# Performance work log

Measured on AMD Instinct MI355X. Metric: run time of the kernel, lower is better.

## Reference

```python
import jax, jax.numpy as jnp
import numpy as np

H = 8          # num heads
HD = 64        # head dim
DV = 512       # values_dim
DC = 128       # coords_dim
DI = 512       # att_inner_dim
DF = 2048      # mlp inner dim


def _ln(x, g, b, eps=1e-5):
    mu = jnp.mean(x, -1, keepdims=True)
    var = jnp.mean((x - mu) ** 2, -1, keepdims=True)
    return (x - mu) * jax.lax.rsqrt(var + eps) * g + b


def _rms(x, g, eps=1e-6):
    return x * jax.lax.rsqrt(jnp.mean(x * x, -1, keepdims=True) + eps) * g


def _heads(x):  # b n (h d) -> b h n d
    b, n, _ = x.shape
    return x.reshape(b, n, H, HD).transpose(0, 2, 1, 3)


def setup_inputs() -> dict:
    key = jax.random.key(0)
    ks = iter(jax.random.split(key, 40))
    r = lambda shape, s=0.02: jax.random.normal(next(ks), shape, jnp.float32) * s
    inp = {
        'coords': jax.random.normal(next(ks), (4, 4096, DC), jnp.float32),
        'values': jax.random.normal(next(ks), (4, 4096, DV), jnp.float32),
        'Lv': jax.random.normal(next(ks), (4, 1024, DV), jnp.float32),
        'Lc': jax.random.normal(next(ks), (4, 1024, DC), jnp.float32),
        'lam': jax.random.normal(next(ks), (1,), jnp.float32),
        'lvn_g': jnp.ones((DV,)), 'lvn_b': jnp.zeros((DV,)),
        'lcn_g': jnp.ones((DC,)), 'lcn_b': jnp.zeros((DC,)),
        'ck_w': r((DC, DI)), 'ck_b': jnp.zeros((DI,)), 'ck_g': jnp.ones((DI,)),
        'cq_w': r((DC, DI)), 'cq_b': jnp.zeros((DI,)), 'cq_g': jnp.ones((DI,)),
        'vq_w': r((DV, DI)), 'vq_b': jnp.zeros((DI,)), 'vq_g': jnp.ones((DI,)),
        'vk_w': r((DV, 2 * DI)), 'vk_b': jnp.zeros((2 * DI,)),
        'op_w': r((DI, DV)), 'op_b': jnp.zeros((DV,)),
        'oln_g': jnp.ones((DV,)), 'oln_b': jnp.zeros((DV,)),
        'm1_w': r((DV, DF)), 'm1_b': jnp.zeros((DF,)),
        'm2_w': r((DF, DF)), 'm2_b': jnp.zeros((DF,)),
        'm3_w': r((DF, DV)), 'm3_b': jnp.zeros((DV,)),
    }
    return inp


def reference(coords, values, Lv, Lc, lam, lvn_g, lvn_b, lcn_g, lcn_b,
              ck_w, ck_b, ck_g, cq_w, cq_b, cq_g, vq_w, vq_b, vq_g,
              vk_w, vk_b, op_w, op_b, oln_g, oln_b,
              m1_w, m1_b, m2_w, m2_b, m3_w, m3_b):
    Lv = _ln(Lv, lvn_g, lvn_b)
    Lc = _ln(Lc, lcn_g, lcn_b)
    vk = Lv @ vk_w + vk_b                     # [b, nl, 2*DI]
    v_v, k_v = jnp.split(vk, 2, axis=-1)
    k_c = _rms(Lc @ ck_w + ck_b, ck_g)
    k_c, v_v, k_v = _heads(k_c), _heads(v_v), _heads(k_v)  # [b,h,nl,d]
    q_v = _heads(_rms(values @ vq_w + vq_b, vq_g))         # [b,h,nq,d]
    q_c = _heads(_rms(coords @ cq_w + cq_b, cq_g))
    # dual-score attention
    scores = jnp.einsum('bhnd,bhmd->bhnm', q_c, k_c) \
        + lam[0] * jnp.einsum('bhnd,bhmd->bhnm', q_v, k_v)
    scores = scores / np.float32(np.sqrt(HD))
    attn = jax.nn.softmax(scores, axis=-1)
    V_out = jnp.einsum('bhnm,bhmd->bhnd', attn, v_v)       # [b,h,nq,d]
    b, _, nq, _ = V_out.shape
    V_out = V_out.transpose(0, 2, 1, 3).reshape(b, nq, DI)
    V_out = V_out @ op_w + op_b
    # (LayerNorm, MLP) head: Linear-GELU-Linear-GELU-Linear
    h = _ln(V_out, oln_g, oln_b)
    h = jax.nn.gelu(h @ m1_w + m1_b)
    h = jax.nn.gelu(h @ m2_w + m2_b)
    return h @ m3_w + m3_b
```

## Files before the change

### kernel.cpp

```cpp
#include <hip/hip_runtime.h>
#include <cstdint>
#include <cstddef>

typedef __bf16 bf16_t;
typedef __bf16 bf16x8 __attribute__((ext_vector_type(8)));
typedef __bf16 bf16x4 __attribute__((ext_vector_type(4)));
typedef float  f32x4  __attribute__((ext_vector_type(4)));

typedef __attribute__((address_space(1))) void gvoid_t;
typedef __attribute__((address_space(3))) void lvoid_t;

__device__ __forceinline__ f32x4 mfma16(bf16x8 a, bf16x8 b, f32x4 c) {
  return __builtin_amdgcn_mfma_f32_16x16x32_bf16(a, b, c, 0, 0, 0);
}

__device__ __forceinline__ void async_copy16(const void* g, void* l) {
  __builtin_amdgcn_global_load_lds((gvoid_t*)g, (lvoid_t*)l, 16, 0, 0);
}

__device__ __forceinline__ float gelu_tanh(float x) {
  float u = 0.7978845608028654f * (x + 0.044715f * x * x * x);
  float e = exp2f(2.8853900817779268f * u);
  float t = 1.f - 2.f / (e + 1.f);
  return 0.5f * x * (1.f + t);
}

struct TransBatch {
  const float* src[8];
  bf16_t* dst[8];
  int K[8], N[8], bx[8], base[8];
};

__global__ void transpose_batch_kernel(TransBatch d) {
  int id = blockIdx.x;
  int mi = 0;
#pragma unroll
  for (int j = 1; j < 8; j++)
    if (id >= d.base[j]) mi = j;
  int local = id - d.base[mi];
  int bxw = d.bx[mi];
  int n0 = (local % bxw) * 32, k0 = (local / bxw) * 32;
  const float* in = d.src[mi];
  bf16_t* out = d.dst[mi];
  int K = d.K[mi], N = d.N[mi];

  __shared__ float t[32][33];
  int tx = threadIdx.x, ty = threadIdx.y;
#pragma unroll
  for (int i = 0; i < 4; i++)
    t[ty + i * 8][tx] = in[(size_t)(k0 + ty + i * 8) * N + n0 + tx];
  __syncthreads();
#pragma unroll
  for (int i = 0; i < 4; i++)
    out[(size_t)(n0 + ty + i * 8) * K + k0 + tx] = (bf16_t)t[tx][ty + i * 8];
}

__global__ void transpose_v_kernel(const bf16_t* __restrict__ vk, bf16_t* __restrict__ vt) {
  __shared__ bf16_t t[32][33];
  int b = blockIdx.z;
  int d0 = blockIdx.x * 32, m0 = blockIdx.y * 32;
  int tx = threadIdx.x, ty = threadIdx.y;
#pragma unroll
  for (int i = 0; i < 4; i++)
    t[ty + i * 8][tx] = vk[((size_t)b * 1024 + m0 + ty + i * 8) * 1024 + d0 + tx];
  __syncthreads();
#pragma unroll
  for (int i = 0; i < 4; i++)
    vt[((size_t)b * 512 + d0 + ty + i * 8) * 1024 + m0 + tx] = t[tx][ty + i * 8];
}

__global__ void cvt2_bf16_kernel(const float* __restrict__ a, bf16_t* __restrict__ oa, int n4a,
                                 const float* __restrict__ b, bf16_t* __restrict__ ob, int n4b) {
  int i = blockIdx.x * blockDim.x + threadIdx.x;
  const float* s;
  bf16_t* o;
  int j;
  if (i < n4a) { s = a; o = oa; j = i; }
  else { j = i - n4a; if (j >= n4b) return; s = b; o = ob; }
  float4 v = ((const float4*)s)[j];
  bf16x4 r = {(bf16_t)v.x, (bf16_t)v.y, (bf16_t)v.z, (bf16_t)v.w};
  ((bf16x4*)o)[j] = r;
}

template <int D>
__global__ void ln_kernel(const float* __restrict__ x, const float* __restrict__ g,
                          const float* __restrict__ bb, bf16_t* __restrict__ out) {
  int row = blockIdx.x, t = threadIdx.x;
  float v = x[(size_t)row * D + t];
  float s = v, s2 = v * v;
#pragma unroll
  for (int o = 32; o > 0; o >>= 1) { s += __shfl_xor(s, o); s2 += __shfl_xor(s2, o); }
  __shared__ float rs[8], rs2[8];
  constexpr int NW = D / 64;
  int w = t >> 6;
  if ((t & 63) == 0) { rs[w] = s; rs2[w] = s2; }
  __syncthreads();
  if (t < 64) {
    float a = (t < NW) ? rs[t] : 0.f;
    float a2 = (t < NW) ? rs2[t] : 0.f;
#pragma unroll
    for (int o = 4; o > 0; o >>= 1) { a += __shfl_xor(a, o); a2 += __shfl_xor(a2, o); }
    if (t == 0) { rs[0] = a; rs2[0] = a2; }
  }
  __syncthreads();
  float mu = rs[0] * (1.f / D);
  float var = rs2[0] * (1.f / D) - mu * mu;
  float rr = rsqrtf(var + 1e-5f);
  out[(size_t)row * D + t] = (bf16_t)((v - mu) * rr * g[t] + bb[t]);
}

__global__ void rms_kernel(const float* __restrict__ x, const float* __restrict__ g,
                           bf16_t* __restrict__ out) {
  int row = blockIdx.x, t = threadIdx.x;
  float v = x[(size_t)row * 512 + t];
  float s2 = v * v;
#pragma unroll
  for (int o = 32; o > 0; o >>= 1) s2 += __shfl_xor(s2, o);
  __shared__ float rs2[8];
  int w = t >> 6;
  if ((t & 63) == 0) rs2[w] = s2;
  __syncthreads();
  if (t < 64) {
    float a = (t < 8) ? rs2[t] : 0.f;
#pragma unroll
    for (int o = 4; o > 0; o >>= 1) a += __shfl_xor(a, o);
    if (t == 0) rs2[0] = a;
  }
  __syncthreads();
  float r = rsqrtf(rs2[0] * (1.f / 512.f) + 1e-6f);
  out[(size_t)row * 512 + t] = (bf16_t)(v * r * g[t]);
}

template <int EPI>
__global__ __launch_bounds__(256, 2) void gemm_bt(
    const bf16_t* __restrict__ A, const bf16_t* __restrict__ Bt,
    const float* __restrict__ bias, void* __restrict__ outp,
    int M, int N, int K) {
  __shared__ __align__(16) bf16_t As[128 * 32];
  __shared__ __align__(16) bf16_t Bs[128 * 32];
  const int tid = threadIdx.x;
  const int lane = tid & 63, wv = tid >> 6;
  const int quad = lane >> 4, l16 = lane & 15;
  const int m_base = blockIdx.y * 128, n_base = blockIdx.x * 128;
  const int wm = wv & 1, wn = wv >> 1;
  f32x4 acc[4][4] = {};

  for (int k0 = 0; k0 < K; k0 += 32) {
#pragma unroll
    for (int c = 0; c < 2; c++) {
      int p = c * 256 + tid;
      int row = p >> 2;
      int kc = (p & 3) ^ ((row >> 1) & 3);
      async_copy16(&A[(size_t)(m_base + row) * K + k0 + kc * 8], &As[(size_t)p * 8]);
      async_copy16(&Bt[(size_t)(n_base + row) * K + k0 + kc * 8], &Bs[(size_t)p * 8]);
    }
    __syncthreads();
    bf16x8 af[4], bfr[4];
#pragma unroll
    for (int mi = 0; mi < 4; mi++) {
      int r = wm * 64 + mi * 16 + l16;
      int kc = quad ^ ((r >> 1) & 3);
      af[mi] = *(const bf16x8*)&As[(size_t)(r * 4 + kc) * 8];
    }
#pragma unroll
    for (int ni = 0; ni < 4; ni++) {
      int r = wn * 64 + ni * 16 + l16;
      int kc = quad ^ ((r >> 1) & 3);
      bfr[ni] = *(const bf16x8*)&Bs[(size_t)(r * 4 + kc) * 8];
    }
#pragma unroll
    for (int mi = 0; mi < 4; mi++)
#pragma unroll
      for (int ni = 0; ni < 4; ni++)
        acc[mi][ni] = mfma16(af[mi], bfr[ni], acc[mi][ni]);
    __syncthreads();
  }

#pragma unroll
  for (int mi = 0; mi < 4; mi++) {
    int m = m_base + wm * 64 + mi * 16 + quad * 4;
#pragma unroll
    for (int ni = 0; ni < 4; ni++) {
      int n = n_base + wn * 64 + ni * 16 + l16;
      float bv = bias[n];
#pragma unroll
      for (int r2 = 0; r2 < 4; r2++) {
        float v = acc[mi][ni][r2] + bv;
        if (EPI == 2) v = gelu_tanh(v);
        if (EPI == 0) ((float*)outp)[(size_t)(m + r2) * N + n] = v;
        else          ((bf16_t*)outp)[(size_t)(m + r2) * N + n] = (bf16_t)v;
      }
    }
  }
}

template <int EPI>
__global__ __launch_bounds__(256, 2) void gemm64(
    const bf16_t* __restrict__ A, const bf16_t* __restrict__ Bt,
    const float* __restrict__ bias, void* __restrict__ outp,
    int M, int N, int K) {
  __shared__ __align__(16) bf16_t As[64 * 32];
  __shared__ __align__(16) bf16_t Bs[128 * 32];
  const int tid = threadIdx.x;
  const int lane = tid & 63, wv = tid >> 6;
  const int quad = lane >> 4, l16 = lane & 15;
  const int m_base = blockIdx.y * 64, n_base = blockIdx.x * 128;
  const int wm = wv & 1, wn = wv >> 1;
  f32x4 acc[2][4] = {};

  for (int k0 = 0; k0 < K; k0 += 32) {
    {
      int p = tid;
      int row = p >> 2;
      int kc = (p & 3) ^ ((row >> 1) & 3);
      async_copy16(&A[(size_t)(m_base + row) * K + k0 + kc * 8], &As[(size_t)p * 8]);
    }
#pragma unroll
    for (int c = 0; c < 2; c++) {
      int p = c * 256 + tid;
      int row = p >> 2;
      int kc = (p & 3) ^ ((row >> 1) & 3);
      async_copy16(&Bt[(size_t)(n_base + row) * K + k0 + kc * 8], &Bs[(size_t)p * 8]);
    }
    __syncthreads();
    bf16x8 af[2], bfr[4];
#pragma unroll
    for (int mi = 0; mi < 2; mi++) {
      int r = wm * 32 + mi * 16 + l16;
      int kc = quad ^ ((r >> 1) & 3);
      af[mi] = *(const bf16x8*)&As[(size_t)(r * 4 + kc) * 8];
    }
#pragma unroll
    for (int ni = 0; ni < 4; ni++) {
      int r = wn * 64 + ni * 16 + l16;
      int kc = quad ^ ((r >> 1) & 3);
      bfr[ni] = *(const bf16x8*)&Bs[(size_t)(r * 4 + kc) * 8];
    }
#pragma unroll
    for (int mi = 0; mi < 2; mi++)
#pragma unroll
      for (int ni = 0; ni < 4; ni++)
        acc[mi][ni] = mfma16(af[mi], bfr[ni], acc[mi][ni]);
    __syncthreads();
  }

#pragma unroll
  for (int mi = 0; mi < 2; mi++) {
    int m = m_base + wm * 32 + mi * 16 + quad * 4;
#pragma unroll
    for (int ni = 0; ni < 4; ni++) {
      int n = n_base + wn * 64 + ni * 16 + l16;
      float bv = bias[n];
#pragma unroll
      for (int r2 = 0; r2 < 4; r2++) {
        float v = acc[mi][ni][r2] + bv;
        if (EPI == 2) v = gelu_tanh(v);
        if (EPI == 0) ((float*)outp)[(size_t)(m + r2) * N + n] = v;
        else          ((bf16_t*)outp)[(size_t)(m + r2) * N + n] = (bf16_t)v;
      }
    }
  }
}

__global__ __launch_bounds__(256, 2) void attn_kernel(
    const bf16_t* __restrict__ qc, const bf16_t* __restrict__ qv,
    const bf16_t* __restrict__ kcb, const bf16_t* __restrict__ vkb,
    const bf16_t* __restrict__ vt, const float* __restrict__ lamp,
    bf16_t* __restrict__ vout) {
  const int b = blockIdx.z, h = blockIdx.y;
  const int tid = threadIdx.x;
  const int lane = tid & 63, wv = tid >> 6;
  const int quad = lane >> 4, l16 = lane & 15;
  const int qrow0 = blockIdx.x * 128 + wv * 32;
  const float SCL = 0.125f * 1.4426950408889634f;
  const float C1 = SCL, C2 = lamp[0] * SCL;

  __shared__ __align__(16) bf16_t kcS[64 * 64];
  __shared__ __align__(16) bf16_t kvS[64 * 64];
  __shared__ __align__(16) bf16_t vtS[64 * 64];
  __shared__ __align__(16) bf16_t sP[4][32 * 64];
  bf16_t* sPw = sP[wv];

  bf16x8 qcf[2][2], qvf[2][2];
#pragma unroll
  for (int mt = 0; mt < 2; mt++)
#pragma unroll
    for (int ks = 0; ks < 2; ks++) {
      size_t o = ((size_t)b * 4096 + qrow0 + mt * 16 + l16) * 512 + h * 64 + ks * 32 + quad * 8;
      qcf[mt][ks] = *(const bf16x8*)&qc[o];
      qvf[mt][ks] = *(const bf16x8*)&qv[o];
    }

  f32x4 O[2][4] = {};
  float ls[2][4] = {};

  for (int kb = 0; kb < 16; kb++) {
#pragma unroll
    for (int i = 0; i < 2; i++) {
      int p = i * 256 + tid;
      int row = p >> 3;
      int gc = (p & 7) ^ (row & 7);
      async_copy16(&kcb[((size_t)b * 1024 + kb * 64 + row) * 512 + h * 64 + gc * 8],
                   &kcS[(size_t)p * 8]);
      async_copy16(&vkb[((size_t)b * 1024 + kb * 64 + row) * 1024 + 512 + h * 64 + gc * 8],
                   &kvS[(size_t)p * 8]);
      async_copy16(&vt[((size_t)((b * 8 + h) * 64) + row) * 1024 + kb * 64 + gc * 8],
                   &vtS[(size_t)p * 8]);
    }
    __syncthreads();

#pragma unroll
    for (int nt = 0; nt < 4; nt++) {
      int krow = nt * 16 + l16;
      int kb8 = krow & 7;
      bf16x8 kc0 = *(const bf16x8*)&kcS[(size_t)(krow * 8 + (quad ^ kb8)) * 8];
      bf16x8 kc1 = *(const bf16x8*)&kcS[(size_t)(krow * 8 + ((4 + quad) ^ kb8)) * 8];
      bf16x8 kv0 = *(const bf16x8*)&kvS[(size_t)(krow * 8 + (quad ^ kb8)) * 8];
      bf16x8 kv1 = *(const bf16x8*)&kvS[(size_t)(krow * 8 + ((4 + quad) ^ kb8)) * 8];
#pragma unroll
      for (int mt = 0; mt < 2; mt++) {
        f32x4 sc = {};
        sc = mfma16(qcf[mt][0], kc0, sc);
        sc = mfma16(qcf[mt][1], kc1, sc);
        f32x4 sv = {};
        sv = mfma16(qvf[mt][0], kv0, sv);
        sv = mfma16(qvf[mt][1], kv1, sv);
#pragma unroll
        for (int r = 0; r < 4; r++) {
          float p = exp2f(sc[r] * C1 + sv[r] * C2);
          ls[mt][r] += p;
          int prow = mt * 16 + quad * 4 + r;
          int col = nt * 16 + l16;
          sPw[prow * 64 + (((col >> 3) ^ (prow & 7)) * 8) + (col & 7)] = (bf16_t)p;
        }
      }
    }
    asm volatile("s_waitcnt lgkmcnt(0)" ::: "memory");

#pragma unroll
    for (int ks2 = 0; ks2 < 2; ks2++) {
      bf16x8 pa[2];
#pragma unroll
      for (int mt = 0; mt < 2; mt++) {
        int prow = mt * 16 + l16;
        pa[mt] = *(const bf16x8*)&sPw[(size_t)(prow * 8 + ((ks2 * 4 + quad) ^ (prow & 7))) * 8];
      }
#pragma unroll
      for (int ntd = 0; ntd < 4; ntd++) {
        int drow = ntd * 16 + l16;
        bf16x8 vb = *(const bf16x8*)&vtS[(size_t)(drow * 8 + ((ks2 * 4 + quad) ^ (drow & 7))) * 8];
        O[0][ntd] = mfma16(pa[0], vb, O[0][ntd]);
        O[1][ntd] = mfma16(pa[1], vb, O[1][ntd]);
      }
    }
    __syncthreads();
  }

#pragma unroll
  for (int mt = 0; mt < 2; mt++) {
    float inv[4];
#pragma unroll
    for (int r = 0; r < 4; r++) {
      float v = ls[mt][r];
      v += __shfl_xor(v, 1);
      v += __shfl_xor(v, 2);
      v += __shfl_xor(v, 4);
      v += __shfl_xor(v, 8);
      inv[r] = 1.f / v;
    }
#pragma unroll
    for (int ntd = 0; ntd < 4; ntd++)
#pragma unroll
      for (int r = 0; r < 4; r++) {
        size_t o = ((size_t)b * 4096 + qrow0 + mt * 16 + quad * 4 + r) * 512 + h * 64 + ntd * 16 + l16;
        vout[o] = (bf16_t)(O[mt][ntd][r] * inv[r]);
      }
  }
}

extern "C" void kernel_launch(void* const* d_in, const int* in_sizes, int n_in,
                              void* d_out, int out_size, void* d_ws, size_t ws_size,
                              hipStream_t stream) {
  (void)in_sizes; (void)n_in; (void)out_size; (void)ws_size;
  const float* coords = (const float*)d_in[0];
  const float* values = (const float*)d_in[1];
  const float* Lv     = (const float*)d_in[2];
  const float* Lc     = (const float*)d_in[3];
  const float* lam    = (const float*)d_in[4];
  const float* lvn_g  = (const float*)d_in[5];
  const float* lvn_b  = (const float*)d_in[6];
  const float* lcn_g  = (const float*)d_in[7];
  const float* lcn_b  = (const float*)d_in[8];
  const float* ck_w = (const float*)d_in[9];  const float* ck_b = (const float*)d_in[10]; const float* ck_g = (const float*)d_in[11];
  const float* cq_w = (const float*)d_in[12]; const float* cq_b = (const float*)d_in[13]; const float* cq_g = (const float*)d_in[14];
  const float* vq_w = (const float*)d_in[15]; const float* vq_b = (const float*)d_in[16]; const float* vq_g = (const float*)d_in[17];
  const float* vk_w = (const float*)d_in[18]; const float* vk_b = (const float*)d_in[19];
  const float* op_w = (const float*)d_in[20]; const float* op_b = (const float*)d_in[21];
  const float* oln_g = (const float*)d_in[22]; const float* oln_b = (const float*)d_in[23];
  const float* m1_w = (const float*)d_in[24]; const float* m1_b = (const float*)d_in[25];
  const float* m2_w = (const float*)d_in[26]; const float* m2_b = (const float*)d_in[27];
  const float* m3_w = (const float*)d_in[28]; const float* m3_b = (const float*)d_in[29];

  char* ws = (char*)d_ws;
  size_t off = 0;
  auto alloc = [&](size_t bytes) { void* p = ws + off; off += (bytes + 255) & ~(size_t)255; return p; };

  bf16_t* wt_m1 = (bf16_t*)alloc((size_t)512 * 2048 * 2);
  bf16_t* wt_m2 = (bf16_t*)alloc((size_t)2048 * 2048 * 2);
  bf16_t* wt_m3 = (bf16_t*)alloc((size_t)2048 * 512 * 2);
  float*  scr0  = (float*) alloc((size_t)16384 * 512 * 4);
  bf16_t* qv_bf = (bf16_t*)alloc((size_t)16384 * 512 * 2);
  bf16_t* qc_bf = (bf16_t*)alloc((size_t)16384 * 512 * 2);
  bf16_t* voutb = (bf16_t*)alloc((size_t)16384 * 512 * 2);
  bf16_t* h0    = (bf16_t*)alloc((size_t)16384 * 512 * 2);
  bf16_t* h1    = (bf16_t*)alloc((size_t)16384 * 2048 * 2);
  bf16_t* h2    = (bf16_t*)alloc((size_t)16384 * 2048 * 2);

  size_t ov = (size_t)((char*)h1 - ws);
  auto oalloc = [&](size_t bytes) { void* p = ws + ov; ov += (bytes + 255) & ~(size_t)255; return p; };
  bf16_t* wt_vk = (bf16_t*)oalloc((size_t)1024 * 512 * 2);
  bf16_t* wt_ck = (bf16_t*)oalloc((size_t)512 * 128 * 2);
  bf16_t* wt_cq = (bf16_t*)oalloc((size_t)512 * 128 * 2);
  bf16_t* wt_vq = (bf16_t*)oalloc((size_t)512 * 512 * 2);
  bf16_t* wt_op = (bf16_t*)oalloc((size_t)512 * 512 * 2);
  bf16_t* lv_ln = (bf16_t*)oalloc((size_t)4096 * 512 * 2);
  bf16_t* lc_ln = (bf16_t*)oalloc((size_t)4096 * 128 * 2);
  bf16_t* vkob  = (bf16_t*)oalloc((size_t)4096 * 1024 * 2);
  float*  kc_f  = (float*) oalloc((size_t)4096 * 512 * 4);
  bf16_t* kc_bf = (bf16_t*)oalloc((size_t)4096 * 512 * 2);
  bf16_t* val_bf= (bf16_t*)oalloc((size_t)16384 * 512 * 2);
  bf16_t* crd_bf= (bf16_t*)oalloc((size_t)16384 * 128 * 2);
  bf16_t* vt    = (bf16_t*)oalloc((size_t)4 * 512 * 1024 * 2);

  TransBatch tb8;
  const float* srcs[8] = {vk_w, ck_w, cq_w, vq_w, op_w, m1_w, m2_w, m3_w};
  bf16_t* dsts[8] = {wt_vk, wt_ck, wt_cq, wt_vq, wt_op, wt_m1, wt_m2, wt_m3};
  int Ks[8] = {512, 128, 128, 512, 512, 512, 2048, 2048};
  int Ns[8] = {1024, 512, 512, 512, 512, 2048, 2048, 512};
  int cum = 0;
  for (int i = 0; i < 8; i++) {
    tb8.src[i] = srcs[i]; tb8.dst[i] = dsts[i];
    tb8.K[i] = Ks[i]; tb8.N[i] = Ns[i];
    tb8.bx[i] = Ns[i] / 32;
    tb8.base[i] = cum;
    cum += (Ns[i] / 32) * (Ks[i] / 32);
  }
  transpose_batch_kernel<<<cum, dim3(32, 8), 0, stream>>>(tb8);

  cvt2_bf16_kernel<<<(16384 * 512 / 4 + 16384 * 128 / 4 + 255) / 256, 256, 0, stream>>>(
      values, val_bf, 16384 * 512 / 4, coords, crd_bf, 16384 * 128 / 4);

  ln_kernel<512><<<4096, 512, 0, stream>>>(Lv, lvn_g, lvn_b, lv_ln);
  ln_kernel<128><<<4096, 128, 0, stream>>>(Lc, lcn_g, lcn_b, lc_ln);

  gemm64<1><<<dim3(8, 64), 256, 0, stream>>>(lv_ln, wt_vk, vk_b, vkob, 4096, 1024, 512);
  gemm64<0><<<dim3(4, 64), 256, 0, stream>>>(lc_ln, wt_ck, ck_b, kc_f, 4096, 512, 128);
  rms_kernel<<<4096, 512, 0, stream>>>(kc_f, ck_g, kc_bf);

  gemm64<0><<<dim3(4, 256), 256, 0, stream>>>(val_bf, wt_vq, vq_b, scr0, 16384, 512, 512);
  rms_kernel<<<16384, 512, 0, stream>>>(scr0, vq_g, qv_bf);
  gemm64<0><<<dim3(4, 256), 256, 0, stream>>>(crd_bf, wt_cq, cq_b, scr0, 16384, 512, 128);
  rms_kernel<<<16384, 512, 0, stream>>>(scr0, cq_g, qc_bf);

  transpose_v_kernel<<<dim3(16, 32, 4), dim3(32, 8), 0, stream>>>(vkob, vt);

  attn_kernel<<<dim3(32, 8, 4), 256, 0, stream>>>(qc_bf, qv_bf, kc_bf, vkob, vt, lam, voutb);

  gemm64<0><<<dim3(4, 256), 256, 0, stream>>>(voutb, wt_op, op_b, scr0, 16384, 512, 512);
  ln_kernel<512><<<16384, 512, 0, stream>>>(scr0, oln_g, oln_b, h0);

  gemm_bt<2><<<dim3(16, 128), 256, 0, stream>>>(h0, wt_m1, m1_b, h1, 16384, 2048, 512);
  gemm_bt<2><<<dim3(16, 128), 256, 0, stream>>>(h1, wt_m2, m2_b, h2, 16384, 2048, 2048);
  gemm64<0><<<dim3(4, 256), 256, 0, stream>>>(h2, wt_m3, m3_b, (float*)d_out, 16384, 512, 2048);
}
```

Before: 700.7 us.

## Deepen gemm_bt K-tile to 64, store intermediates in bf16, route m3 to gemm_bt

The 128x128 gemm_bt kernel now stages a 64-wide K slice per barrier, using an 8-chunk XOR swizzle, so each synchronisation covers two MFMA k-steps. Intermediate pre-norm GEMM outputs (q/k projections, output projection) are written as bf16 instead of fp32, and the norm kernels are templated to read bf16, which cuts memory traffic. The final m3 projection moves from the 64-tile kernel to the larger-tile gemm_bt. The trade-offs are doubled LDS per block, which may reduce occupancy, and extra bf16 rounding before the RMS/LayerNorm steps.

Result: faster. 673.8 us (-3.8%).

```diff
diff --git a/kernel.cpp b/kernel.cpp
--- a/kernel.cpp
+++ b/kernel.cpp
@@ -82,11 +82,11 @@
   ((bf16x4*)o)[j] = r;
 }
 
-template <int D>
-__global__ void ln_kernel(const float* __restrict__ x, const float* __restrict__ g,
+template <int D, typename TI>
+__global__ void ln_kernel(const TI* __restrict__ x, const float* __restrict__ g,
                           const float* __restrict__ bb, bf16_t* __restrict__ out) {
   int row = blockIdx.x, t = threadIdx.x;
-  float v = x[(size_t)row * D + t];
+  float v = (float)x[(size_t)row * D + t];
   float s = v, s2 = v * v;
 #pragma unroll
   for (int o = 32; o > 0; o >>= 1) { s += __shfl_xor(s, o); s2 += __shfl_xor(s2, o); }
@@ -109,10 +109,11 @@
   out[(size_t)row * D + t] = (bf16_t)((v - mu) * rr * g[t] + bb[t]);
 }
 
-__global__ void rms_kernel(const float* __restrict__ x, const float* __restrict__ g,
+template <typename TI>
+__global__ void rms_kernel(const TI* __restrict__ x, const float* __restrict__ g,
                            bf16_t* __restrict__ out) {
   int row = blockIdx.x, t = threadIdx.x;
-  float v = x[(size_t)row * 512 + t];
+  float v = (float)x[(size_t)row * 512 + t];
   float s2 = v * v;
 #pragma unroll
   for (int o = 32; o > 0; o >>= 1) s2 += __shfl_xor(s2, o);
@@ -136,8 +137,8 @@
     const bf16_t* __restrict__ A, const bf16_t* __restrict__ Bt,
     const float* __restrict__ bias, void* __restrict__ outp,
     int M, int N, int K) {
-  __shared__ __align__(16) bf16_t As[128 * 32];
-  __shared__ __align__(16) bf16_t Bs[128 * 32];
+  __shared__ __align__(16) bf16_t As[128 * 64];
+  __shared__ __align__(16) bf16_t Bs[128 * 64];
   const int tid = threadIdx.x;
   const int lane = tid & 63, wv = tid >> 6;
   const int quad = lane >> 4, l16 = lane & 15;
@@ -145,34 +146,37 @@
   const int wm = wv & 1, wn = wv >> 1;
   f32x4 acc[4][4] = {};
 
-  for (int k0 = 0; k0 < K; k0 += 32) {
-#pragma unroll
-    for (int c = 0; c < 2; c++) {
+  for (int k0 = 0; k0 < K; k0 += 64) {
+#pragma unroll
+    for (int c = 0; c < 4; c++) {
       int p = c * 256 + tid;
-      int row = p >> 2;
-      int kc = (p & 3) ^ ((row >> 1) & 3);
-      async_copy16(&A[(size_t)(m_base + row) * K + k0 + kc * 8], &As[(size_t)p * 8]);
-      async_copy16(&Bt[(size_t)(n_base + row) * K + k0 + kc * 8], &Bs[(size_t)p * 8]);
-    }
-    __syncthreads();
-    bf16x8 af[4], bfr[4];
-#pragma unroll
-    for (int mi = 0; mi < 4; mi++) {
-      int r = wm * 64 + mi * 16 + l16;
-      int kc = quad ^ ((r >> 1) & 3);
-      af[mi] = *(const bf16x8*)&As[(size_t)(r * 4 + kc) * 8];
-    }
-#pragma unroll
-    for (int ni = 0; ni < 4; ni++) {
-      int r = wn * 64 + ni * 16 + l16;
-      int kc = quad ^ ((r >> 1) & 3);
-      bfr[ni] = *(const bf16x8*)&Bs[(size_t)(r * 4 + kc) * 8];
-    }
-#pragma unroll
-    for (int mi = 0; mi < 4; mi++)
-#pragma unroll
-      for (int ni = 0; ni < 4; ni++)
-        acc[mi][ni] = mfma16(af[mi], bfr[ni], acc[mi][ni]);
+      int row = p >> 3;
+      int gc = (p & 7) ^ (row & 7);
+      async_copy16(&A[(size_t)(m_base + row) * K + k0 + gc * 8], &As[(size_t)p * 8]);
+      async_copy16(&Bt[(size_t)(n_base + row) * K + k0 + gc * 8], &Bs[(size_t)p * 8]);
+    }
+    __syncthreads();
+#pragma unroll
+    for (int ks = 0; ks < 2; ks++) {
+      bf16x8 af[4], bfr[4];
+#pragma unroll
+      for (int mi = 0; mi < 4; mi++) {
+        int r = wm * 64 + mi * 16 + l16;
+        int c = (ks * 4 + quad) ^ (r & 7);
+        af[mi] = *(const bf16x8*)&As[(size_t)(r * 8 + c) * 8];
+      }
+#pragma unroll
+      for (int ni = 0; ni < 4; ni++) {
+        int r = wn * 64 + ni * 16 + l16;
+        int c = (ks * 4 + quad) ^ (r & 7);
+        bfr[ni] = *(const bf16x8*)&Bs[(size_t)(r * 8 + c) * 8];
+      }
+#pragma unroll
+      for (int mi = 0; mi < 4; mi++)
+#pragma unroll
+        for (int ni = 0; ni < 4; ni++)
+          acc[mi][ni] = mfma16(af[mi], bfr[ni], acc[mi][ni]);
+    }
     __syncthreads();
   }
 
@@ -408,7 +412,7 @@
   bf16_t* wt_m1 = (bf16_t*)alloc((size_t)512 * 2048 * 2);
   bf16_t* wt_m2 = (bf16_t*)alloc((size_t)2048 * 2048 * 2);
   bf16_t* wt_m3 = (bf16_t*)alloc((size_t)2048 * 512 * 2);
-  float*  scr0  = (float*) alloc((size_t)16384 * 512 * 4);
+  bf16_t* scr0  = (bf16_t*)alloc((size_t)16384 * 512 * 4);
   bf16_t* qv_bf = (bf16_t*)alloc((size_t)16384 * 512 * 2);
   bf16_t* qc_bf = (bf16_t*)alloc((size_t)16384 * 512 * 2);
   bf16_t* voutb = (bf16_t*)alloc((size_t)16384 * 512 * 2);
@@ -426,7 +430,7 @@
   bf16_t* lv_ln = (bf16_t*)oalloc((size_t)4096 * 512 * 2);
   bf16_t* lc_ln = (bf16_t*)oalloc((size_t)4096 * 128 * 2);
   bf16_t* vkob  = (bf16_t*)oalloc((size_t)4096 * 1024 * 2);
-  float*  kc_f  = (float*) oalloc((size_t)4096 * 512 * 4);
+  bf16_t* kc_b  = (bf16_t*)oalloc((size_t)4096 * 512 * 2);
   bf16_t* kc_bf = (bf16_t*)oalloc((size_t)4096 * 512 * 2);
   bf16_t* val_bf= (bf16_t*)oalloc((size_t)16384 * 512 * 2);
   bf16_t* crd_bf= (bf16_t*)oalloc((size_t)16384 * 128 * 2);
@@ -450,26 +454,26 @@
   cvt2_bf16_kernel<<<(16384 * 512 / 4 + 16384 * 128 / 4 + 255) / 256, 256, 0, stream>>>(
       values, val_bf, 16384 * 512 / 4, coords, crd_bf, 16384 * 128 / 4);
 
-  ln_kernel<512><<<4096, 512, 0, stream>>>(Lv, lvn_g, lvn_b, lv_ln);
-  ln_kernel<128><<<4096, 128, 0, stream>>>(Lc, lcn_g, lcn_b, lc_ln);
+  ln_kernel<512, float><<<4096, 512, 0, stream>>>(Lv, lvn_g, lvn_b, lv_ln);
+  ln_kernel<128, float><<<4096, 128, 0, stream>>>(Lc, lcn_g, lcn_b, lc_ln);
 
   gemm64<1><<<dim3(8, 64), 256, 0, stream>>>(lv_ln, wt_vk, vk_b, vkob, 4096, 1024, 512);
-  gemm64<0><<<dim3(4, 64), 256, 0, stream>>>(lc_ln, wt_ck, ck_b, kc_f, 4096, 512, 128);
-  rms_kernel<<<4096, 512, 0, stream>>>(kc_f, ck_g, kc_bf);
-
-  gemm64<0><<<dim3(4, 256), 256, 0, stream>>>(val_bf, wt_vq, vq_b, scr0, 16384, 512, 512);
-  rms_kernel<<<16384, 512, 0, stream>>>(scr0, vq_g, qv_bf);
-  gemm64<0><<<dim3(4, 256), 256, 0, stream>>>(crd_bf, wt_cq, cq_b, scr0, 16384, 512, 128);
-  rms_kernel<<<16384, 512, 0, stream>>>(scr0, cq_g, qc_bf);
+  gemm64<1><<<dim3(4, 64), 256, 0, stream>>>(lc_ln, wt_ck, ck_b, kc_b, 4096, 512, 128);
+  rms_kernel<bf16_t><<<4096, 512, 0, stream>>>(kc_b, ck_g, kc_bf);
+
+  gemm64<1><<<dim3(4, 256), 256, 0, stream>>>(val_bf, wt_vq, vq_b, scr0, 16384, 512, 512);
+  rms_kernel<bf16_t><<<16384, 512, 0, stream>>>(scr0, vq_g, qv_bf);
+  gemm64<1><<<dim3(4, 256), 256, 0, stream>>>(crd_bf, wt_cq, cq_b, scr0, 16384, 512, 128);
+  rms_kernel<bf16_t><<<16384, 512, 0, stream>>>(scr0, cq_g, qc_bf);
 
   transpose_v_kernel<<<dim3(16, 32, 4), dim3(32, 8), 0, stream>>>(vkob, vt);
 
   attn_kernel<<<dim3(32, 8, 4), 256, 0, stream>>>(qc_bf, qv_bf, kc_bf, vkob, vt, lam, voutb);
 
-  gemm64<0><<<dim3(4, 256), 256, 0, stream>>>(voutb, wt_op, op_b, scr0, 16384, 512, 512);
-  ln_kernel<512><<<16384, 512, 0, stream>>>(scr0, oln_g, oln_b, h0);
+  gemm64<1><<<dim3(4, 256), 256, 0, stream>>>(voutb, wt_op, op_b, scr0, 16384, 512, 512);
+  ln_kernel<512, bf16_t><<<16384, 512, 0, stream>>>(scr0, oln_g, oln_b, h0);
 
   gemm_bt<2><<<dim3(16, 128), 256, 0, stream>>>(h0, wt_m1, m1_b, h1, 16384, 2048, 512);
   gemm_bt<2><<<dim3(16, 128), 256, 0, stream>>>(h1, wt_m2, m2_b, h2, 16384, 2048, 2048);
-  gemm64<0><<<dim3(4, 256), 256, 0, stream>>>(h2, wt_m3, m3_b, (float*)d_out, 16384, 512, 2048);
-}
+  gemm_bt<0><<<dim3(4, 128), 256, 0, stream>>>(h2, wt_m3, m3_b, (float*)d_out, 16384, 512, 2048);
+}
```
